# Performance work log

Hardware: AMD Instinct MI355X
Metric: run time of the kernel (lower is better)

Reference implementation:

```python
import jax, jax.numpy as jnp
import numpy as np
import math

DIM = 1024
H = 16          # num_heads
DH = 64         # dim_head
FD = 32         # feature_dim = int(0.5 * dim_head)
B = 4
S = 4096
EPS = 1e-8


def setup_inputs() -> dict:
    key = jax.random.key(0)
    ks = jax.random.split(key, 10)
    inner = H * DH
    x = jax.random.normal(ks[0], (B, S, DIM), dtype=jnp.float32)
    # Linear weights stored as [in, out] (transposed torch layout), small init scale
    Wq = jax.random.normal(ks[1], (DIM, inner), dtype=jnp.float32) * 0.02
    bq = jnp.zeros((inner,), dtype=jnp.float32)
    Wk = jax.random.normal(ks[2], (DIM, inner), dtype=jnp.float32) * 0.02
    bk = jnp.zeros((inner,), dtype=jnp.float32)
    Wv = jax.random.normal(ks[3], (DIM, inner), dtype=jnp.float32) * 0.02
    bv = jnp.zeros((inner,), dtype=jnp.float32)
    Wo = jax.random.normal(ks[4], (inner, DIM), dtype=jnp.float32) * 0.02
    bo = jnp.zeros((DIM,), dtype=jnp.float32)
    # proj_matrix buffer: QR of randn(dim_head, feature_dim), scaled by sqrt(dim_head)
    rm = np.asarray(jax.random.normal(ks[5], (DH, FD), dtype=jnp.float32))
    q_orth, _ = np.linalg.qr(rm)
    proj = jnp.asarray(q_orth, dtype=jnp.float32) * math.sqrt(DH)
    return {"x": x, "Wq": Wq, "bq": bq, "Wk": Wk, "bk": bk,
            "Wv": Wv, "bv": bv, "proj": proj, "Wo": Wo, "bo": bo}


def _heads(t, b, n):
    # [b, n, H*DH] -> [b, H, n, DH]
    return t.reshape(b, n, H, DH).transpose(0, 2, 1, 3)


def reference(x, Wq, bq, Wk, bk, Wv, bv, proj, Wo, bo):
    b, n, _ = x.shape
    q = _heads(x @ Wq + bq, b, n)   # bhnd
    k = _heads(x @ Wk + bk, b, n)
    v = _heads(x @ Wv + bv, b, n)
    inv_sqrt_f = 1.0 / math.sqrt(FD)
    q_prime = jax.nn.relu(jnp.einsum('bhnd,df->bhnf', q, proj)) * inv_sqrt_f
    k_prime = jax.nn.relu(jnp.einsum('bhnd,df->bhnf', k, proj)) * inv_sqrt_f
    kv = jnp.einsum('bhnf,bhnd->bhfd', k_prime, v)          # [b,h,FD,DH]
    z = 1.0 / (jnp.einsum('bhnf,bhf->bhn', q_prime, k_prime.sum(axis=2)) + EPS)
    attn = jnp.einsum('bhnf,bhfd->bhnd', q_prime, kv) * z[..., None]
    attn = attn.transpose(0, 2, 1, 3).reshape(b, n, H * DH)
    return attn @ Wo + bo            # dropout in eval mode = identity
```

## Files before the change

kernel.cpp:

```cpp
#include <hip/hip_runtime.h>

typedef unsigned short u16;
typedef __attribute__((ext_vector_type(8))) short bf16x8;
typedef __attribute__((ext_vector_type(4))) float f32x4;

__device__ inline float bf2f(u16 u) {
    unsigned v = ((unsigned)u) << 16;
    return __builtin_bit_cast(float, v);
}
__device__ inline u16 f2bf(float f) {
    unsigned u = __builtin_bit_cast(unsigned, f);
    u += 0x7fff + ((u >> 16) & 1);
    return (u16)(u >> 16);
}

__device__ inline void gload_lds16(const void* g, void* l) {
    __builtin_amdgcn_global_load_lds(
        (const __attribute__((address_space(1))) unsigned int*)(unsigned long long)g,
        (__attribute__((address_space(3))) unsigned int*)(unsigned)(unsigned long long)l,
        16, 0, 0);
}

__global__ __launch_bounds__(256) void prep(
    const float4* __restrict__ x, bf16x8* __restrict__ xb,
    const float* __restrict__ Wq, const float* __restrict__ Wk,
    const float* __restrict__ bq, const float* __restrict__ bk,
    const float* __restrict__ proj,
    const float* __restrict__ Wv, const float* __restrict__ Wo,
    const float* __restrict__ bv,
    u16* __restrict__ WallT, u16* __restrict__ WoT, float* __restrict__ bias_all)
{
    __shared__ float smem[10240];
    const int bid = blockIdx.x;
    const int tid = threadIdx.x;

    if (bid < 8192) {
        long i = (long)bid * 256 + tid;
        float4 v0 = x[2 * i];
        float4 v1 = x[2 * i + 1];
        bf16x8 o;
        o[0] = (short)f2bf(v0.x); o[1] = (short)f2bf(v0.y);
        o[2] = (short)f2bf(v0.z); o[3] = (short)f2bf(v0.w);
        o[4] = (short)f2bf(v1.x); o[5] = (short)f2bf(v1.y);
        o[6] = (short)f2bf(v1.z); o[7] = (short)f2bf(v1.w);
        xb[i] = o;
    } else if (bid < 8448) {
        const int fb = bid - 8192;
        const int qk = fb >> 7, h = (fb >> 3) & 15, kt = fb & 7;
        const float* W  = qk ? Wk : Wq;
        const float* bb = qk ? bk : bq;
        const int kin0 = kt * 128;
        float* pj    = smem;
        float* panel = smem + 2048;
        {
            const float4* ps = (const float4*)proj;
            float4* pd = (float4*)pj;
            #pragma unroll
            for (int it = 0; it < 2; ++it) pd[it * 256 + tid] = ps[it * 256 + tid];
        }
        #pragma unroll
        for (int it = 0; it < 8; ++it) {
            const int li = it * 256 + tid;
            const int row = li >> 4, c4 = (li & 15) * 4;
            *(float4*)&panel[row * 64 + c4] =
                *(const float4*)&W[(long)(kin0 + row) * 1024 + h * 64 + c4];
        }
        __syncthreads();

        const int f = tid & 31, g = tid >> 5;
        float pjr[64];
        #pragma unroll
        for (int d = 0; d < 64; ++d) pjr[d] = pj[d * 32 + f];

        alignas(16) u16 outv[16];
        #pragma unroll
        for (int rr = 0; rr < 16; ++rr) {
            const float4* prow = (const float4*)&panel[(g * 16 + rr) * 64];
            float acc = 0.f;
            #pragma unroll
            for (int d4 = 0; d4 < 16; ++d4) {
                float4 p = prow[d4];
                acc += p.x * pjr[d4 * 4]     + p.y * pjr[d4 * 4 + 1]
                     + p.z * pjr[d4 * 4 + 2] + p.w * pjr[d4 * 4 + 3];
            }
            outv[rr] = f2bf(acc);
        }
        u16* dst = WallT + (long)(qk * 512 + h * 32 + f) * 1024 + kin0 + g * 16;
        *(bf16x8*)dst     = *(const bf16x8*)&outv[0];
        *(bf16x8*)&dst[8] = *(const bf16x8*)&outv[8];

        if (kt == 0 && g == 0) {
            float a = 0.f;
            #pragma unroll
            for (int d = 0; d < 64; ++d) a += bb[h * 64 + d] * pjr[d];
            bias_all[qk * 512 + h * 32 + f] = a;
        }
    } else {
        const int tb = bid - 8448;
        const bool isV = (tb < 256);
        const int tile = isV ? tb : (tb - 256);
        const int kt = tile >> 4, ct = tile & 15;
        const float* src = isV ? Wv : Wo;
        float* T = smem;
        #pragma unroll
        for (int it = 0; it < 16; ++it) {
            const int kl = it * 4 + (tid >> 6);
            T[kl * 65 + (tid & 63)] = src[(long)(kt * 64 + kl) * 1024 + ct * 64 + (tid & 63)];
        }
        __syncthreads();
        #pragma unroll
        for (int it = 0; it < 2; ++it) {
            const int li = it * 256 + tid;
            const int cl = li >> 3, k8 = (li & 7) * 8;
            bf16x8 o;
            #pragma unroll
            for (int j = 0; j < 8; ++j) o[j] = (short)f2bf(T[(k8 + j) * 65 + cl]);
            u16* dst = isV ? (WallT + (long)(1024 + ct * 64 + cl) * 1024)
                           : (WoT   + (long)(ct * 64 + cl) * 1024);
            *(bf16x8*)&dst[kt * 64 + k8] = o;
        }
        if (isV && kt == 0 && tid < 64) bias_all[1024 + ct * 64 + tid] = bv[ct * 64 + tid];
    }
}

template<int NBN, bool RELUQK, typename OutT>
__global__ __launch_bounds__(512, 2) void gemm256(
    const u16* __restrict__ A, const u16* __restrict__ Bt,
    const float* __restrict__ bias, OutT* __restrict__ C, long moff)
{
    constexpr int NCOLS = NBN * 256;
    __shared__ alignas(16) u16 lds[65536];

    const int bid = blockIdx.x;
    const int wg  = (bid & 7) * ((int)gridDim.x >> 3) + (bid >> 3);
    const long m0 = moff + (long)(wg / NBN) * 256;
    const long n0 = (long)(wg % NBN) * 256;

    const int tid  = threadIdx.x;
    const int wave = tid >> 6, lane = tid & 63;
    const int wm = wave >> 2, wn = wave & 3;

    const int srow = wave * 32 + (lane >> 2);
    const int gch  = ((lane & 3) ^ ((lane >> 3) & 3)) * 8;
    const u16* pA0 = A  + (m0 + srow) * 1024 + gch;
    const u16* pA1 = pA0 + 16 * 1024;
    const u16* pB0 = Bt + (n0 + srow) * 1024 + gch;
    const u16* pB1 = pB0 + 16 * 1024;

    #define SUB(b_,kh_,ab_) (lds + (((b_)*2+(kh_))*2+(ab_))*8192)
    #define STG_A(b_,kh_,t_) { const int k0_ = (t_)*64 + (kh_)*32;            \
        u16* d_ = SUB(b_,kh_,0) + wave * 1024;                                \
        gload_lds16(pA0 + k0_, d_); gload_lds16(pA1 + k0_, d_ + 512); }
    #define STG_B(b_,kh_,t_) { const int k0_ = (t_)*64 + (kh_)*32;            \
        u16* d_ = SUB(b_,kh_,1) + wave * 1024;                                \
        gload_lds16(pB0 + k0_, d_); gload_lds16(pB1 + k0_, d_ + 512); }

    const int m  = lane & 15, kc = lane >> 4;
    const int off  = (kc ^ ((m >> 1) & 3)) * 8;
    const int arow = (wm * 128 + m) * 32 + off;
    const int brow = (wn * 64  + m) * 32 + off;

    f32x4  acc[8][4] = {};
    bf16x8 af[8];
    bf16x8 b0, b1;

    #define DSA(b_,kh_) { const u16* s_ = SUB(b_,kh_,0);                      \
        _Pragma("unroll") for (int mt_ = 0; mt_ < 8; ++mt_)                   \
            af[mt_] = *(const bf16x8*)(s_ + arow + mt_ * 512); }
    #define DSB(b_,kh_,nh_) { const u16* s_ = SUB(b_,kh_,1) + brow + (nh_)*1024; \
        b0 = *(const bf16x8*)(s_); b1 = *(const bf16x8*)(s_ + 512); }
    #define MM(nh_) { _Pragma("unroll") for (int mt_ = 0; mt_ < 8; ++mt_) {   \
        acc[mt_][(nh_)*2]   = __builtin_amdgcn_mfma_f32_16x16x32_bf16(        \
            af[mt_], b0, acc[mt_][(nh_)*2],   0, 0, 0);                       \
        acc[mt_][(nh_)*2+1] = __builtin_amdgcn_mfma_f32_16x16x32_bf16(        \
            af[mt_], b1, acc[mt_][(nh_)*2+1], 0, 0, 0); } }
    #define BARMM(nh_)                                                        \
        __builtin_amdgcn_s_barrier();                                         \
        asm volatile("s_waitcnt lgkmcnt(0)" ::: "memory");                    \
        __builtin_amdgcn_s_setprio(1);                                        \
        MM(nh_);                                                              \
        __builtin_amdgcn_s_setprio(0);                                        \
        __builtin_amdgcn_s_barrier();

    STG_A(0,0,0); STG_B(0,0,0);
    STG_A(0,1,0); STG_B(0,1,0);
    STG_A(1,0,1); STG_B(1,0,1);
    asm volatile("s_waitcnt vmcnt(4)" ::: "memory");
    __builtin_amdgcn_s_barrier();

    #pragma unroll 1
    for (int i = 0; i < 8; ++i) {
        const int  t1   = 2 * i + 1;
        const bool more = (i < 7);
        DSA(0,0); DSB(0,0,0);
        STG_A(1,1,t1);
        BARMM(0);
        DSB(0,0,1);
        STG_B(1,1,t1);
        BARMM(1);
        DSA(0,1); DSB(0,1,0);
        if (more) STG_A(0,0,t1+1);
        BARMM(0);
        DSB(0,1,1);
        if (more) {
            STG_B(0,0,t1+1);
            asm volatile("s_waitcnt vmcnt(4)" ::: "memory");
        } else {
            asm volatile("s_waitcnt vmcnt(0)" ::: "memory");
        }
        BARMM(1);
        DSA(1,0); DSB(1,0,0);
        if (more) STG_A(0,1,t1+1);
        BARMM(0);
        DSB(1,0,1);
        if (more) STG_B(0,1,t1+1);
        BARMM(1);
        DSA(1,1); DSB(1,1,0);
        if (more) STG_A(1,0,t1+2);
        BARMM(0);
        DSB(1,1,1);
        if (more) {
            STG_B(1,0,t1+2);
            asm volatile("s_waitcnt vmcnt(4)" ::: "memory");
        }
        BARMM(1);
    }

    if constexpr (sizeof(OutT) == 2) {
        const bool dorelu = RELUQK && (n0 < 1024);
        #pragma unroll
        for (int nf = 0; nf < 4; ++nf) {
            const int col = wn * 64 + nf * 16 + m;
            const float bval = bias[n0 + col];
            #pragma unroll
            for (int mt = 0; mt < 8; ++mt) {
                #pragma unroll
                for (int r = 0; r < 4; ++r) {
                    const int row = wm * 128 + mt * 16 + kc * 4 + r;
                    float c = acc[mt][nf][r] + bval;
                    if (dorelu) c = fmaxf(c, 0.f) * 0.17677669529663687f;
                    const int x = ((row >> 2) & 7) << 1;
                    lds[row * 256 + (((col >> 3) ^ x) << 3) + (col & 7)] = f2bf(c);
                }
            }
        }
        __syncthreads();
        #pragma unroll
        for (int it = 0; it < 16; ++it) {
            const int li = it * 512 + tid;
            const int row = li >> 5, ch = li & 31;
            const int x = ((row >> 2) & 7) << 1;
            bf16x8 v = *(const bf16x8*)&lds[row * 256 + ((ch ^ x) << 3)];
            *(bf16x8*)&C[(m0 + row) * (long)NCOLS + n0 + ch * 8] = v;
        }
    } else {
        float* ft = (float*)lds;
        #pragma unroll 1
        for (int half = 0; half < 2; ++half) {
            __syncthreads();
            if (wm == half) {
                #pragma unroll
                for (int nf = 0; nf < 4; ++nf) {
                    const int col = wn * 64 + nf * 16 + m;
                    const float bval = bias[n0 + col];
                    #pragma unroll
                    for (int mt = 0; mt < 8; ++mt) {
                        #pragma unroll
                        for (int r = 0; r < 4; ++r) {
                            const int row = mt * 16 + kc * 4 + r;
                            const int x = ((row >> 2) & 7) << 1;
                            ft[row * 256 + (((col >> 2) ^ x) << 2) + (col & 3)] =
                                acc[mt][nf][r] + bval;
                        }
                    }
                }
            }
            __syncthreads();
            #pragma unroll
            for (int it = 0; it < 16; ++it) {
                const int li = it * 512 + tid;
                const int row = li >> 6, ch = li & 63;
                const int x = ((row >> 2) & 7) << 1;
                float4 v = *(const float4*)&ft[row * 256 + ((ch ^ x) << 2)];
                *(float4*)&C[(m0 + half * 128 + row) * (long)NCOLS + n0 + ch * 4] = v;
            }
        }
    }
    #undef SUB
    #undef STG_A
    #undef STG_B
    #undef DSA
    #undef DSB
    #undef MM
    #undef BARMM
}

__global__ __launch_bounds__(256) void kv_v3(const u16* __restrict__ Y,
                                             float* __restrict__ part_kv,
                                             float* __restrict__ part_ks)
{
    __shared__ float ksf[128 * 33];
    __shared__ float vsf[128 * 68];
    const int bh = blockIdx.x, c = blockIdx.y;
    const int b = bh >> 4, h = bh & 15;
    const int tid = threadIdx.x;
    const long rbase = (long)b * 4096 + (long)c * 128;

    #pragma unroll
    for (int it = 0; it < 2; ++it) {
        const int lr = it * 64 + (tid >> 2), cc = (tid & 3) * 8;
        bf16x8 kx = *(const bf16x8*)(Y + (rbase + lr) * 2048 + 512 + h * 32 + cc);
        #pragma unroll
        for (int j = 0; j < 8; ++j) ksf[lr * 33 + cc + j] = bf2f((u16)kx[j]);
    }
    #pragma unroll
    for (int it = 0; it < 4; ++it) {
        const int lr = it * 32 + (tid >> 3), cc = (tid & 7) * 8;
        bf16x8 vx = *(const bf16x8*)(Y + (rbase + lr) * 2048 + 1024 + h * 64 + cc);
        #pragma unroll
        for (int j = 0; j < 8; ++j) vsf[lr * 68 + cc + j] = bf2f((u16)vx[j]);
    }
    __syncthreads();

    const int f = tid >> 3, dg = (tid & 7) * 8;
    float acc[8] = {};
    float ksacc = 0.f;
    #pragma unroll 4
    for (int n = 0; n < 128; ++n) {
        const float kf = ksf[n * 33 + f];
        const float4 v0 = *(const float4*)&vsf[n * 68 + dg];
        const float4 v1 = *(const float4*)&vsf[n * 68 + dg + 4];
        acc[0] += kf * v0.x; acc[1] += kf * v0.y;
        acc[2] += kf * v0.z; acc[3] += kf * v0.w;
        acc[4] += kf * v1.x; acc[5] += kf * v1.y;
        acc[6] += kf * v1.z; acc[7] += kf * v1.w;
        ksacc += kf;
    }

    float* o = part_kv + (((long)bh * 32 + c) * 32 + f) * 64 + dg;
    *(f32x4*)o       = f32x4{acc[0], acc[1], acc[2], acc[3]};
    *(f32x4*)(o + 4) = f32x4{acc[4], acc[5], acc[6], acc[7]};
    if ((tid & 7) == 0) part_ks[(bh * 32 + c) * 32 + f] = ksacc;
}

__global__ __launch_bounds__(256) void kv_reduce(const float* __restrict__ part_kv,
                                                 const float* __restrict__ part_ks,
                                                 float* __restrict__ kv,
                                                 float* __restrict__ ksum)
{
    const int idx = blockIdx.x * 256 + threadIdx.x;
    if (blockIdx.x < 512) {
        const int bh = idx >> 11, off = idx & 2047;
        const float* p = part_kv + (long)bh * 65536 + off;
        float s = 0.f;
        #pragma unroll 8
        for (int c = 0; c < 32; c++) s += p[c * 2048];
        kv[idx] = s;
    } else {
        const int i2 = idx - 512 * 256;
        const int bh = i2 >> 5, f = i2 & 31;
        const float* p = part_ks + bh * 1024 + f;
        float s = 0.f;
        #pragma unroll 8
        for (int c = 0; c < 32; c++) s += p[c * 32];
        ksum[i2] = s;
    }
}

__global__ __launch_bounds__(256) void attn_v2(const u16* __restrict__ Y,
                                               const float* __restrict__ kv,
                                               const float* __restrict__ ksum,
                                               u16* __restrict__ attn)
{
    __shared__ float qsf[64 * 36];
    __shared__ float kss[32];
    __shared__ float zs[64];
    const int tid = threadIdx.x;
    const int bh = blockIdx.x;
    const int b = bh >> 4, h = bh & 15;
    const long row0 = (long)b * 4096 + (long)blockIdx.y * 64;

    {
        const int lr = tid >> 2, c8 = (tid & 3) * 8;
        bf16x8 qx = *(const bf16x8*)(Y + (row0 + lr) * 2048 + h * 32 + c8);
        #pragma unroll
        for (int j = 0; j < 8; ++j) qsf[lr * 36 + c8 + j] = bf2f((u16)qx[j]);
    }
    if (tid < 32) kss[tid] = ksum[bh * 32 + tid];

    const int wave = tid >> 6, lane = tid & 63;
    const float* kvg = kv + (long)bh * 2048 + lane;
    float kvreg[32];
    #pragma unroll
    for (int ff = 0; ff < 32; ++ff) kvreg[ff] = kvg[ff * 64];

    __syncthreads();

    {
        const int lr = wave * 16 + (lane & 15);
        float den = 0.f;
        #pragma unroll
        for (int fc = 0; fc < 8; ++fc) {
            const float4 q = *(const float4*)&qsf[lr * 36 + fc * 4];
            den += q.x * kss[fc * 4]     + q.y * kss[fc * 4 + 1]
                 + q.z * kss[fc * 4 + 2] + q.w * kss[fc * 4 + 3];
        }
        if (lane < 16) zs[lr] = 1.f / (den + 1e-8f);
    }
    __syncthreads();

    #pragma unroll
    for (int rg = 0; rg < 4; ++rg) {
        const int lr0 = wave * 16 + rg * 4;
        float acc0 = 0.f, acc1 = 0.f, acc2 = 0.f, acc3 = 0.f;
        #pragma unroll
        for (int fc = 0; fc < 8; ++fc) {
            const float4 q0 = *(const float4*)&qsf[(lr0 + 0) * 36 + fc * 4];
            const float4 q1 = *(const float4*)&qsf[(lr0 + 1) * 36 + fc * 4];
            const float4 q2 = *(const float4*)&qsf[(lr0 + 2) * 36 + fc * 4];
            const float4 q3 = *(const float4*)&qsf[(lr0 + 3) * 36 + fc * 4];
            const float k0 = kvreg[fc * 4], k1 = kvreg[fc * 4 + 1];
            const float k2 = kvreg[fc * 4 + 2], k3 = kvreg[fc * 4 + 3];
            acc0 += q0.x * k0 + q0.y * k1 + q0.z * k2 + q0.w * k3;
            acc1 += q1.x * k0 + q1.y * k1 + q1.z * k2 + q1.w * k3;
            acc2 += q2.x * k0 + q2.y * k1 + q2.z * k2 + q2.w * k3;
            acc3 += q3.x * k0 + q3.y * k1 + q3.z * k2 + q3.w * k3;
        }
        u16* op = attn + (row0 + lr0) * 1024 + h * 64 + lane;
        op[0]        = f2bf(acc0 * zs[lr0 + 0]);
        op[1024]     = f2bf(acc1 * zs[lr0 + 1]);
        op[2 * 1024] = f2bf(acc2 * zs[lr0 + 2]);
        op[3 * 1024] = f2bf(acc3 * zs[lr0 + 3]);
    }
}

extern "C" void kernel_launch(void* const* d_in, const int* in_sizes, int n_in,
                              void* d_out, int out_size, void* d_ws, size_t ws_size,
                              hipStream_t stream)
{
    const float* x    = (const float*)d_in[0];
    const float* Wq   = (const float*)d_in[1];
    const float* bq   = (const float*)d_in[2];
    const float* Wk   = (const float*)d_in[3];
    const float* bk   = (const float*)d_in[4];
    const float* Wv   = (const float*)d_in[5];
    const float* bv   = (const float*)d_in[6];
    const float* proj = (const float*)d_in[7];
    const float* Wo   = (const float*)d_in[8];
    const float* bo   = (const float*)d_in[9];

    char* w = (char*)d_ws;
    u16*   xbf     = (u16*)  (w);
    float* part_kv = (float*)(w);
    u16*   attn    = (u16*)  (w);
    u16*   wallT   = (u16*)  (w + 33554432);
    u16*   woT     = (u16*)  (w + 37748736);
    float* bias    = (float*)(w + 39845888);
    float* kv      = (float*)(w + 39854080);
    float* ksum    = (float*)(w + 40378368);
    u16*   Y       = (u16*)  (w + 40386560);
    float* part_ks = (float*)(w + 107495424);

    prep<<<8960, 256, 0, stream>>>((const float4*)x, (bf16x8*)xbf,
                                   Wq, Wk, bq, bk, proj, Wv, Wo, bv,
                                   wallT, woT, bias);

    gemm256<8, true, u16><<<256, 512, 0, stream>>>(xbf, wallT, bias, Y, 0L);
    gemm256<8, true, u16><<<256, 512, 0, stream>>>(xbf, wallT, bias, Y, 8192L);

    kv_v3<<<dim3(64, 32), 256, 0, stream>>>(Y, part_kv, part_ks);

    kv_reduce<<<520, 256, 0, stream>>>(part_kv, part_ks, kv, ksum);

    attn_v2<<<dim3(64, 64), 256, 0, stream>>>(Y, kv, ksum, attn);

    gemm256<4, false, float><<<256, 512, 0, stream>>>(attn, woT, bo, (float*)d_out, 0L);
}
```

Before: 315.6 us.

## Fold kv into Wo per batch-head and shrink the output GEMM to K=512

Reassociates attn@Wo as (z·q')·(kv@Wo), precomputing a per-batch matrix G = kv·Wo[h] (512×1024 per batch) with a new gmat kernel. The attention kernel becomes a lightweight z-scaled q' writer (zq_k), and the final GEMM runs with K=512 against per-batch B matrices instead of K=1024. It also merges the two half-M QKV GEMM launches into one 512-block launch and drops the Wo transpose from prep. The trade is an extra small kernel and per-batch weight reads in the last GEMM, plus a different bf16 rounding point.

```diff
diff --git a/kernel.cpp b/kernel.cpp
--- a/kernel.cpp
+++ b/kernel.cpp
@@ -26,9 +26,8 @@
     const float* __restrict__ Wq, const float* __restrict__ Wk,
     const float* __restrict__ bq, const float* __restrict__ bk,
     const float* __restrict__ proj,
-    const float* __restrict__ Wv, const float* __restrict__ Wo,
-    const float* __restrict__ bv,
-    u16* __restrict__ WallT, u16* __restrict__ WoT, float* __restrict__ bias_all)
+    const float* __restrict__ Wv, const float* __restrict__ bv,
+    u16* __restrict__ WallT, float* __restrict__ bias_all)
 {
     __shared__ float smem[10240];
     const int bid = blockIdx.x;
@@ -96,16 +95,13 @@
             bias_all[qk * 512 + h * 32 + f] = a;
         }
     } else {
-        const int tb = bid - 8448;
-        const bool isV = (tb < 256);
-        const int tile = isV ? tb : (tb - 256);
+        const int tile = bid - 8448;
         const int kt = tile >> 4, ct = tile & 15;
-        const float* src = isV ? Wv : Wo;
         float* T = smem;
         #pragma unroll
         for (int it = 0; it < 16; ++it) {
             const int kl = it * 4 + (tid >> 6);
-            T[kl * 65 + (tid & 63)] = src[(long)(kt * 64 + kl) * 1024 + ct * 64 + (tid & 63)];
+            T[kl * 65 + (tid & 63)] = Wv[(long)(kt * 64 + kl) * 1024 + ct * 64 + (tid & 63)];
         }
         __syncthreads();
         #pragma unroll
@@ -115,37 +111,40 @@
             bf16x8 o;
             #pragma unroll
             for (int j = 0; j < 8; ++j) o[j] = (short)f2bf(T[(k8 + j) * 65 + cl]);
-            u16* dst = isV ? (WallT + (long)(1024 + ct * 64 + cl) * 1024)
-                           : (WoT   + (long)(ct * 64 + cl) * 1024);
+            u16* dst = WallT + (long)(1024 + ct * 64 + cl) * 1024;
             *(bf16x8*)&dst[kt * 64 + k8] = o;
         }
-        if (isV && kt == 0 && tid < 64) bias_all[1024 + ct * 64 + tid] = bv[ct * 64 + tid];
-    }
-}
-
-template<int NBN, bool RELUQK, typename OutT>
+        if (kt == 0 && tid < 64) bias_all[1024 + ct * 64 + tid] = bv[ct * 64 + tid];
+    }
+}
+
+template<int NBN, bool RELUQK, typename OutT, int KDIM, bool PERBATCH>
 __global__ __launch_bounds__(512, 2) void gemm256(
     const u16* __restrict__ A, const u16* __restrict__ Bt,
-    const float* __restrict__ bias, OutT* __restrict__ C, long moff)
-{
+    const float* __restrict__ bias, OutT* __restrict__ C)
+{
+    constexpr int NWG   = 64 * NBN;
     constexpr int NCOLS = NBN * 256;
+    constexpr int ITERS = KDIM / 128;
     __shared__ alignas(16) u16 lds[65536];
 
     const int bid = blockIdx.x;
-    const int wg  = (bid & 7) * ((int)gridDim.x >> 3) + (bid >> 3);
-    const long m0 = moff + (long)(wg / NBN) * 256;
+    const int wg  = (bid & 7) * (NWG / 8) + (bid >> 3);
+    const long m0 = (long)(wg / NBN) * 256;
     const long n0 = (long)(wg % NBN) * 256;
 
     const int tid  = threadIdx.x;
     const int wave = tid >> 6, lane = tid & 63;
     const int wm = wave >> 2, wn = wave & 3;
 
+    const u16* Btb = PERBATCH ? (Bt + (m0 >> 12) * (long)(1024 * KDIM)) : Bt;
+
     const int srow = wave * 32 + (lane >> 2);
     const int gch  = ((lane & 3) ^ ((lane >> 3) & 3)) * 8;
-    const u16* pA0 = A  + (m0 + srow) * 1024 + gch;
-    const u16* pA1 = pA0 + 16 * 1024;
-    const u16* pB0 = Bt + (n0 + srow) * 1024 + gch;
-    const u16* pB1 = pB0 + 16 * 1024;
+    const u16* pA0 = A   + (m0 + srow) * KDIM + gch;
+    const u16* pA1 = pA0 + 16 * KDIM;
+    const u16* pB0 = Btb + (n0 + srow) * KDIM + gch;
+    const u16* pB1 = pB0 + 16 * KDIM;
 
     #define SUB(b_,kh_,ab_) (lds + (((b_)*2+(kh_))*2+(ab_))*8192)
     #define STG_A(b_,kh_,t_) { const int k0_ = (t_)*64 + (kh_)*32;            \
@@ -189,9 +188,9 @@
     __builtin_amdgcn_s_barrier();
 
     #pragma unroll 1
-    for (int i = 0; i < 8; ++i) {
+    for (int i = 0; i < ITERS; ++i) {
         const int  t1   = 2 * i + 1;
-        const bool more = (i < 7);
+        const bool more = (i < ITERS - 1);
         DSA(0,0); DSB(0,0,0);
         STG_A(1,1,t1);
         BARMM(0);
@@ -367,10 +366,58 @@
     }
 }
 
-__global__ __launch_bounds__(256) void attn_v2(const u16* __restrict__ Y,
-                                               const float* __restrict__ kv,
-                                               const float* __restrict__ ksum,
-                                               u16* __restrict__ attn)
+__global__ __launch_bounds__(256) void gmat(const float* __restrict__ kv,
+                                            const float* __restrict__ Wo,
+                                            u16* __restrict__ GT)
+{
+    __shared__ float kvl[2048];
+    __shared__ float wol[64 * 256];
+    const int bid = blockIdx.x, tid = threadIdx.x;
+    const int bh = bid >> 2, n0 = (bid & 3) * 256;
+    const int b = bh >> 4, h = bh & 15;
+
+    {
+        const float4* s = (const float4*)(kv + (long)bh * 2048);
+        float4* d = (float4*)kvl;
+        d[tid] = s[tid];
+        d[256 + tid] = s[256 + tid];
+    }
+    #pragma unroll
+    for (int it = 0; it < 16; ++it) {
+        const int li = it * 256 + tid;
+        const int row = li >> 6, c4 = (li & 63) * 4;
+        *(float4*)&wol[row * 256 + c4] =
+            *(const float4*)&Wo[(long)(h * 64 + row) * 1024 + n0 + c4];
+    }
+    __syncthreads();
+
+    float out[32] = {};
+    #pragma unroll
+    for (int d4 = 0; d4 < 16; ++d4) {
+        const float w0 = wol[(d4 * 4 + 0) * 256 + tid];
+        const float w1 = wol[(d4 * 4 + 1) * 256 + tid];
+        const float w2 = wol[(d4 * 4 + 2) * 256 + tid];
+        const float w3 = wol[(d4 * 4 + 3) * 256 + tid];
+        #pragma unroll
+        for (int f = 0; f < 32; ++f) {
+            const float4 kq = *(const float4*)&kvl[f * 64 + d4 * 4];
+            out[f] += kq.x * w0 + kq.y * w1 + kq.z * w2 + kq.w * w3;
+        }
+    }
+
+    u16* dst = GT + ((long)b * 1024 + n0 + tid) * 512 + h * 32;
+    #pragma unroll
+    for (int q8 = 0; q8 < 4; ++q8) {
+        bf16x8 o;
+        #pragma unroll
+        for (int j = 0; j < 8; ++j) o[j] = (short)f2bf(out[q8 * 8 + j]);
+        *(bf16x8*)&dst[q8 * 8] = o;
+    }
+}
+
+__global__ __launch_bounds__(256) void zq_k(const u16* __restrict__ Y,
+                                            const float* __restrict__ ksum,
+                                            u16* __restrict__ zq)
 {
     __shared__ float qsf[64 * 36];
     __shared__ float kss[32];
@@ -380,58 +427,34 @@
     const int b = bh >> 4, h = bh & 15;
     const long row0 = (long)b * 4096 + (long)blockIdx.y * 64;
 
+    const int lr = tid >> 2, c8 = (tid & 3) * 8;
     {
-        const int lr = tid >> 2, c8 = (tid & 3) * 8;
         bf16x8 qx = *(const bf16x8*)(Y + (row0 + lr) * 2048 + h * 32 + c8);
         #pragma unroll
         for (int j = 0; j < 8; ++j) qsf[lr * 36 + c8 + j] = bf2f((u16)qx[j]);
     }
     if (tid < 32) kss[tid] = ksum[bh * 32 + tid];
-
-    const int wave = tid >> 6, lane = tid & 63;
-    const float* kvg = kv + (long)bh * 2048 + lane;
-    float kvreg[32];
-    #pragma unroll
-    for (int ff = 0; ff < 32; ++ff) kvreg[ff] = kvg[ff * 64];
-
     __syncthreads();
 
     {
-        const int lr = wave * 16 + (lane & 15);
+        const int wave = tid >> 6, lane = tid & 63;
+        const int r = wave * 16 + (lane & 15);
         float den = 0.f;
         #pragma unroll
         for (int fc = 0; fc < 8; ++fc) {
-            const float4 q = *(const float4*)&qsf[lr * 36 + fc * 4];
+            const float4 q = *(const float4*)&qsf[r * 36 + fc * 4];
             den += q.x * kss[fc * 4]     + q.y * kss[fc * 4 + 1]
                  + q.z * kss[fc * 4 + 2] + q.w * kss[fc * 4 + 3];
         }
-        if (lane < 16) zs[lr] = 1.f / (den + 1e-8f);
+        if (lane < 16) zs[r] = 1.f / (den + 1e-8f);
     }
     __syncthreads();
 
+    const float z = zs[lr];
+    bf16x8 o;
     #pragma unroll
-    for (int rg = 0; rg < 4; ++rg) {
-        const int lr0 = wave * 16 + rg * 4;
-        float acc0 = 0.f, acc1 = 0.f, acc2 = 0.f, acc3 = 0.f;
-        #pragma unroll
-        for (int fc = 0; fc < 8; ++fc) {
-            const float4 q0 = *(const float4*)&qsf[(lr0 + 0) * 36 + fc * 4];
-            const float4 q1 = *(const float4*)&qsf[(lr0 + 1) * 36 + fc * 4];
-            const float4 q2 = *(const float4*)&qsf[(lr0 + 2) * 36 + fc * 4];
-            const float4 q3 = *(const float4*)&qsf[(lr0 + 3) * 36 + fc * 4];
-            const float k0 = kvreg[fc * 4], k1 = kvreg[fc * 4 + 1];
-            const float k2 = kvreg[fc * 4 + 2], k3 = kvreg[fc * 4 + 3];
-            acc0 += q0.x * k0 + q0.y * k1 + q0.z * k2 + q0.w * k3;
-            acc1 += q1.x * k0 + q1.y * k1 + q1.z * k2 + q1.w * k3;
-            acc2 += q2.x * k0 + q2.y * k1 + q2.z * k2 + q2.w * k3;
-            acc3 += q3.x * k0 + q3.y * k1 + q3.z * k2 + q3.w * k3;
-        }
-        u16* op = attn + (row0 + lr0) * 1024 + h * 64 + lane;
-        op[0]        = f2bf(acc0 * zs[lr0 + 0]);
-        op[1024]     = f2bf(acc1 * zs[lr0 + 1]);
-        op[2 * 1024] = f2bf(acc2 * zs[lr0 + 2]);
-        op[3 * 1024] = f2bf(acc3 * zs[lr0 + 3]);
-    }
+    for (int j = 0; j < 8; ++j) o[j] = (short)f2bf(qsf[lr * 36 + c8 + j] * z);
+    *(bf16x8*)&zq[(row0 + lr) * 512 + h * 32 + c8] = o;
 }
 
 extern "C" void kernel_launch(void* const* d_in, const int* in_sizes, int n_in,
@@ -452,27 +475,28 @@
     char* w = (char*)d_ws;
     u16*   xbf     = (u16*)  (w);
     float* part_kv = (float*)(w);
-    u16*   attn    = (u16*)  (w);
+    u16*   zqb     = (u16*)  (w);
+    u16*   GT      = (u16*)  (w + 16777216);
     u16*   wallT   = (u16*)  (w + 33554432);
-    u16*   woT     = (u16*)  (w + 37748736);
     float* bias    = (float*)(w + 39845888);
     float* kv      = (float*)(w + 39854080);
     float* ksum    = (float*)(w + 40378368);
     u16*   Y       = (u16*)  (w + 40386560);
     float* part_ks = (float*)(w + 107495424);
 
-    prep<<<8960, 256, 0, stream>>>((const float4*)x, (bf16x8*)xbf,
-                                   Wq, Wk, bq, bk, proj, Wv, Wo, bv,
-                                   wallT, woT, bias);
-
-    gemm256<8, true, u16><<<256, 512, 0, stream>>>(xbf, wallT, bias, Y, 0L);
-    gemm256<8, true, u16><<<256, 512, 0, stream>>>(xbf, wallT, bias, Y, 8192L);
+    prep<<<8704, 256, 0, stream>>>((const float4*)x, (bf16x8*)xbf,
+                                   Wq, Wk, bq, bk, proj, Wv, bv,
+                                   wallT, bias);
+
+    gemm256<8, true, u16, 1024, false><<<512, 512, 0, stream>>>(xbf, wallT, bias, Y);
 
     kv_v3<<<dim3(64, 32), 256, 0, stream>>>(Y, part_kv, part_ks);
 
     kv_reduce<<<520, 256, 0, stream>>>(part_kv, part_ks, kv, ksum);
 
-    attn_v2<<<dim3(64, 64), 256, 0, stream>>>(Y, kv, ksum, attn);
-
-    gemm256<4, false, float><<<256, 512, 0, stream>>>(attn, woT, bo, (float*)d_out, 0L);
-}
+    gmat<<<256, 256, 0, stream>>>(kv, Wo, GT);
+
+    zq_k<<<dim3(64, 64), 256, 0, stream>>>(Y, ksum, zqb);
+
+    gemm256<4, false, float, 512, true><<<256, 512, 0, stream>>>(zqb, GT, bo, (float*)d_out);
+}
```

New measurement: 308.3 us. 1.02x faster.
